# Performance work log

Measured on AMD Instinct MI355X. Metric: run time of the kernel, lower is better.

Reference implementation:

```python
import jax, jax.numpy as jnp
import numpy as np

B, S, DM, H = 4, 2048, 512, 8
HD = DM // H


def setup_inputs() -> dict:
    key = jax.random.key(0)
    ks = jax.random.split(key, 12)
    x = jax.random.normal(ks[0], (B, S, DM), dtype=jnp.float32)
    # causal lower-triangular mask [B, S, S]
    mask = jnp.broadcast_to(jnp.tril(jnp.ones((S, S), dtype=jnp.int32)), (B, S, S))
    # sorted irregular day offsets (trading-day-like), in days
    days_offset = jnp.sort(
        jax.random.uniform(ks[1], (B, S), dtype=jnp.float32) * 3000.0, axis=-1
    )
    scale = 1.0 / np.sqrt(DM)
    Wq = jax.random.normal(ks[2], (DM, DM), dtype=jnp.float32) * scale
    bq = jnp.zeros((DM,), dtype=jnp.float32)
    Wk = jax.random.normal(ks[3], (DM, DM), dtype=jnp.float32) * scale
    bk = jnp.zeros((DM,), dtype=jnp.float32)
    Wv = jax.random.normal(ks[4], (DM, DM), dtype=jnp.float32) * scale
    bv = jnp.zeros((DM,), dtype=jnp.float32)
    Wo = jax.random.normal(ks[5], (DM, DM), dtype=jnp.float32) * scale
    bo = jnp.zeros((DM,), dtype=jnp.float32)
    decay_rate = jnp.float32(0.1)
    return {
        "x": x, "mask": mask, "days_offset": days_offset,
        "Wq": Wq, "bq": bq, "Wk": Wk, "bk": bk,
        "Wv": Wv, "bv": bv, "Wo": Wo, "bo": bo,
        "decay_rate": decay_rate,
    }


def reference(x, mask, days_offset, Wq, bq, Wk, bk, Wv, bv, Wo, bo, decay_rate):
    b, s, _ = x.shape
    # projections (torch Linear: x @ W.T + b), split heads -> [b, h, s, hd]
    def proj(W, bias):
        return (x @ W.T + bias).reshape(b, s, H, HD).transpose(0, 2, 1, 3)
    q, k, v = proj(Wq, bq), proj(Wk, bk), proj(Wv, bv)
    scores = jnp.einsum("bhqd,bhkd->bhqk", q, k) / jnp.sqrt(jnp.float32(HD))
    # temporal decay: exp(-rate * |t_i - t_j|), broadcast over heads
    dist = jnp.abs(days_offset[:, :, None] - days_offset[:, None, :])  # [b,s,s]
    decay = jnp.exp(-decay_rate * dist)
    scores = scores * decay[:, None, :, :]
    scores = jnp.where(mask[:, None, :, :] == 0, -jnp.inf, scores)
    attn = jax.nn.softmax(scores, axis=-1)  # dropout p=0 (eval)
    out = jnp.einsum("bhqk,bhkd->bhqd", attn, v)
    out = out.transpose(0, 2, 1, 3).reshape(b, s, DM)
    return out @ Wo.T + bo
```

## Files before the change

### kernel.cpp

```cpp
#include <hip/hip_runtime.h>
#include <hip/hip_fp16.h>


#define S_LEN 2048
#define DMODEL 512
#define NH 8
#define HD 64

typedef _Float16 half8 __attribute__((ext_vector_type(8)));
typedef _Float16 half4 __attribute__((ext_vector_type(4)));
typedef float floatx4 __attribute__((ext_vector_type(4)));

__device__ __forceinline__ void gload16(const _Float16* g, _Float16* l) {
    __builtin_amdgcn_global_load_lds(
        (const __attribute__((address_space(1))) void*)g,
        (__attribute__((address_space(3))) void*)l, 16, 0, 0);
}

__device__ __forceinline__ half8 cvt8(float4 a, float4 b) {
    half8 h;
    h[0] = (_Float16)a.x; h[1] = (_Float16)a.y; h[2] = (_Float16)a.z; h[3] = (_Float16)a.w;
    h[4] = (_Float16)b.x; h[5] = (_Float16)b.y; h[6] = (_Float16)b.z; h[7] = (_Float16)b.w;
    return h;
}

__device__ __forceinline__ void stage_f32(
    const float* __restrict__ src, _Float16* __restrict__ dstbase,
    int row, int sw, int lane7, int kcol)
{
    const float* p = src + (size_t)row * DMODEL + kcol + sw * 8;
    float4 a = *(const float4*)p;
    float4 b = *(const float4*)(p + 4);
    *(half8*)(dstbase + row * 64 + lane7 * 8) = cvt8(a, b);
}

__global__ __launch_bounds__(256) void qkv_gemm(
    const float* __restrict__ x,
    const float* __restrict__ Wq, const float* __restrict__ Wk, const float* __restrict__ Wv,
    const float* __restrict__ bq, const float* __restrict__ bk, const float* __restrict__ bv,
    _Float16* __restrict__ outh)
{
    __shared__ _Float16 As[2][128 * 64];
    __shared__ _Float16 Ws[2][128 * 64];
    const int t = threadIdx.x;
    const int bm = blockIdx.x, bn = blockIdx.y, z = blockIdx.z;
    const float* Wp = (z == 0) ? Wq : (z == 1) ? Wk : Wv;
    const float* bias = (z == 0) ? bq : (z == 1) ? bk : bv;
    const int w = t >> 6, lane = t & 63, l15 = lane & 15, quad = lane >> 4;
    const int wrow = (w >> 1) * 64, wcol = (w & 1) * 64;
    const int lrow = lane >> 3, lane7 = lane & 7;
    const int sw = lane7 ^ lrow;
    const float* xb = x  + (size_t)(bm * 128) * DMODEL;
    const float* Wb = Wp + (size_t)(bn * 128) * DMODEL;

    auto stage = [&](int kb, int buf) {
        #pragma unroll
        for (int i = 0; i < 4; ++i) {
            int row = w * 32 + i * 8 + lrow;
            stage_f32(xb, As[buf], row, sw, lane7, kb * 64);
            stage_f32(Wb, Ws[buf], row, sw, lane7, kb * 64);
        }
    };

    floatx4 acc[4][4] = {};
    stage(0, 0);
    for (int kb = 0; kb < 8; ++kb) {
        const int buf = kb & 1;
        __syncthreads();
        if (kb < 7) stage(kb + 1, buf ^ 1);
        #pragma unroll
        for (int kk = 0; kk < 2; ++kk) {
            half8 xf[4], wf[4];
            #pragma unroll
            for (int mt = 0; mt < 4; ++mt)
                xf[mt] = *(const half8*)(&As[buf][(wrow + mt * 16 + l15) * 64 + (((quad + 4 * kk) ^ (l15 & 7)) * 8)]);
            #pragma unroll
            for (int nt = 0; nt < 4; ++nt)
                wf[nt] = *(const half8*)(&Ws[buf][(wcol + nt * 16 + l15) * 64 + (((quad + 4 * kk) ^ (l15 & 7)) * 8)]);
            if (z == 2) {
                #pragma unroll
                for (int mt = 0; mt < 4; ++mt)
                    #pragma unroll
                    for (int nt = 0; nt < 4; ++nt)
                        acc[mt][nt] = __builtin_amdgcn_mfma_f32_16x16x32_f16(xf[mt], wf[nt], acc[mt][nt], 0, 0, 0);
            } else {
                #pragma unroll
                for (int nt = 0; nt < 4; ++nt)
                    #pragma unroll
                    for (int mt = 0; mt < 4; ++mt)
                        acc[nt][mt] = __builtin_amdgcn_mfma_f32_16x16x32_f16(wf[nt], xf[mt], acc[nt][mt], 0, 0, 0);
            }
        }
    }

    if (z == 2) {
        #pragma unroll
        for (int mt = 0; mt < 4; ++mt)
            #pragma unroll
            for (int nt = 0; nt < 4; ++nt) {
                int n = bn * 128 + wcol + nt * 16 + l15;
                float bvv = bias[n];
                int m0 = bm * 128 + wrow + mt * 16 + quad * 4;
                int b = m0 >> 11, s0 = m0 & 2047;
                int hh = n >> 6, hd = n & 63;
                half4 hv;
                #pragma unroll
                for (int r = 0; r < 4; ++r) hv[r] = (_Float16)(acc[mt][nt][r] + bvv);
                *(half4*)(outh + (size_t)2 * (8192 * 512) +
                          ((size_t)(b * NH + hh) * HD + hd) * S_LEN + s0) = hv;
            }
    } else {
        #pragma unroll
        for (int nt = 0; nt < 4; ++nt)
            #pragma unroll
            for (int mt = 0; mt < 4; ++mt) {
                int n0 = bn * 128 + wcol + nt * 16 + quad * 4;
                float4 b4 = *(const float4*)(bias + n0);
                int m = bm * 128 + wrow + mt * 16 + l15;
                int b = m >> 11, s = m & 2047;
                int hh = n0 >> 6, hd0 = n0 & 63;
                half4 hv;
                hv[0] = (_Float16)(acc[nt][mt][0] + b4.x);
                hv[1] = (_Float16)(acc[nt][mt][1] + b4.y);
                hv[2] = (_Float16)(acc[nt][mt][2] + b4.z);
                hv[3] = (_Float16)(acc[nt][mt][3] + b4.w);
                *(half4*)(outh + (size_t)z * (8192 * 512) +
                          ((size_t)(b * NH + hh) * S_LEN + s) * HD + hd0) = hv;
            }
    }
}

__global__ __launch_bounds__(256) void out_gemm(
    const _Float16* __restrict__ A, const float* __restrict__ Wo,
    const float* __restrict__ bo, float* __restrict__ outf)
{
    __shared__ _Float16 As[2][64 * 64];
    __shared__ _Float16 Ws[2][128 * 64];
    const int t = threadIdx.x;
    const int bm = blockIdx.x, bn = blockIdx.y;
    const int w = t >> 6, lane = t & 63, l15 = lane & 15, quad = lane >> 4;
    const int wn = w * 32;
    const int lrow = lane >> 3, lane7 = lane & 7;
    const int sw = lane7 ^ lrow;
    const _Float16* Ab = A  + (size_t)(bm * 64) * DMODEL;
    const float*    Wb = Wo + (size_t)(bn * 128) * DMODEL;

    auto stage = [&](int kb, int buf) {
        #pragma unroll
        for (int i = 0; i < 2; ++i) {
            int row = (w * 2 + i) * 8 + lrow;
            gload16(Ab + (size_t)row * DMODEL + kb * 64 + sw * 8, &As[buf][row * 64]);
        }
        #pragma unroll
        for (int i = 0; i < 4; ++i)
            stage_f32(Wb, Ws[buf], w * 32 + i * 8 + lrow, sw, lane7, kb * 64);
    };

    floatx4 acc[2][4] = {};
    stage(0, 0);
    for (int kb = 0; kb < 8; ++kb) {
        const int buf = kb & 1;
        __syncthreads();
        if (kb < 7) stage(kb + 1, buf ^ 1);
        #pragma unroll
        for (int kk = 0; kk < 2; ++kk) {
            half8 wf[2], af[4];
            #pragma unroll
            for (int nt = 0; nt < 2; ++nt)
                wf[nt] = *(const half8*)(&Ws[buf][(wn + nt * 16 + l15) * 64 + (((quad + 4 * kk) ^ (l15 & 7)) * 8)]);
            #pragma unroll
            for (int mt = 0; mt < 4; ++mt)
                af[mt] = *(const half8*)(&As[buf][(mt * 16 + l15) * 64 + (((quad + 4 * kk) ^ (l15 & 7)) * 8)]);
            #pragma unroll
            for (int nt = 0; nt < 2; ++nt)
                #pragma unroll
                for (int mt = 0; mt < 4; ++mt)
                    acc[nt][mt] = __builtin_amdgcn_mfma_f32_16x16x32_f16(wf[nt], af[mt], acc[nt][mt], 0, 0, 0);
        }
    }

    #pragma unroll
    for (int nt = 0; nt < 2; ++nt)
        #pragma unroll
        for (int mt = 0; mt < 4; ++mt) {
            int n0 = bn * 128 + wn + nt * 16 + quad * 4;
            float4 b4 = *(const float4*)(bo + n0);
            int m = bm * 64 + mt * 16 + l15;
            float4 v;
            v.x = acc[nt][mt][0] + b4.x; v.y = acc[nt][mt][1] + b4.y;
            v.z = acc[nt][mt][2] + b4.z; v.w = acc[nt][mt][3] + b4.w;
            *(float4*)(outf + (size_t)m * DMODEL + n0) = v;
        }
}

__global__ __launch_bounds__(256, 3) void attn_k(
    const _Float16* __restrict__ Qh, const _Float16* __restrict__ Kh,
    const _Float16* __restrict__ Vt, const float* __restrict__ days,
    const float* __restrict__ rate_p, _Float16* __restrict__ Ah)
{
    __shared__ _Float16 Ks[2][64 * 64];
    __shared__ _Float16 Vs[2][64 * 64];
    __shared__ float    eks[2][64];
    __shared__ float4   PsRaw[1024];
    __shared__ float    lred[2][2][64];

    _Float16* Ps  = (_Float16*)PsRaw;
    float*    PsF = (float*)PsRaw;

    const int h = blockIdx.x, b = blockIdx.z;
    const int j = 31 - blockIdx.y;
    const int t = threadIdx.x, w = t >> 6, lane = t & 63;
    const int l15 = lane & 15, quad = lane >> 4, e7 = l15 & 7;
    const int qh = w & 1, kh = w >> 1;
    const float rate = rate_p[0];
    const size_t bhoff = (size_t)(b * NH + h) * (size_t)(S_LEN * HD);
    const _Float16* Qb = Qh + bhoff;
    const _Float16* Kb = Kh + bhoff;
    const _Float16* Vb = Vt + bhoff;
    const float* daysb = days + b * S_LEN;
    const int lrow = lane >> 3, sw = (lane & 7) ^ lrow;

    auto stage = [&](int kt, int buf) {
        #pragma unroll
        for (int i = 0; i < 2; ++i) {
            int grp = w * 2 + i;
            int row = grp * 8 + lrow;
            gload16(Kb + (size_t)(kt * 64 + row) * HD + sw * 8, &Ks[buf][grp * 512]);
            gload16(Vb + (size_t)row * S_LEN + kt * 64 + sw * 8, &Vs[buf][grp * 512]);
        }
        if (w == 0) {
            float tk0 = daysb[kt * 64];
            float d = daysb[kt * 64 + lane];
            eks[buf][lane] = __expf(fminf(rate * (d - tk0), 80.f));
        }
    };

    const int q0 = j * 64 + qh * 32;
    half8 qf[2][2];
    #pragma unroll
    for (int qc = 0; qc < 2; ++qc)
        #pragma unroll
        for (int kk = 0; kk < 2; ++kk)
            qf[qc][kk] = *(const half8*)(Qb + (size_t)(q0 + qc * 16 + l15) * HD + kk * 32 + quad * 8);

    const int   qg[2] = {q0 + l15, q0 + 16 + l15};
    const float tq[2] = {daysb[qg[0]], daysb[qg[1]]};

    floatx4 oacc[2][4] = {};
    float lacc[2] = {0.f, 0.f};

    floatx4 scA[2][2], scB[2][2];
    half8  vfA[4], vfB[4];
    floatx4 ekA[2], ekB[2];
    float  eqA[2], eqB[2];

    auto load_tile = [&](int kt, int par, floatx4 (&sc)[2][2], half8 (&vf)[4],
                         floatx4 (&ek)[2], float (&eq)[2]) {
        half8 kf[2][2];
        #pragma unroll
        for (int c = 0; c < 2; ++c) {
            const int C = kh * 2 + c;
            #pragma unroll
            for (int kk = 0; kk < 2; ++kk)
                kf[c][kk] = *(const half8*)(&Ks[par][(C * 16 + l15) * 64 + (((quad + 4 * kk) ^ e7) * 8)]);
        }
        #pragma unroll
        for (int qc = 0; qc < 2; ++qc)
            #pragma unroll
            for (int c = 0; c < 2; ++c) {
                floatx4 z = {};
                z = __builtin_amdgcn_mfma_f32_16x16x32_f16(kf[c][0], qf[qc][0], z, 0, 0, 0);
                sc[qc][c] = __builtin_amdgcn_mfma_f32_16x16x32_f16(kf[c][1], qf[qc][1], z, 0, 0, 0);
            }
        #pragma unroll
        for (int s4 = 0; s4 < 4; ++s4)
            vf[s4] = *(const half8*)(&Vs[par][(s4 * 16 + l15) * 64 + (((quad + 4 * kh) ^ e7) * 8)]);
        const float tk0 = daysb[kt * 64];
        #pragma unroll
        for (int qc = 0; qc < 2; ++qc)
            eq[qc] = 0.125f * __expf(-rate * (tq[qc] - tk0));
        #pragma unroll
        for (int c = 0; c < 2; ++c)
            ek[c] = *(const floatx4*)(&eks[par][kh * 32 + c * 16 + quad * 4]);
    };

    auto softmax_pv = [&](floatx4 (&sc)[2][2], half8 (&vf)[4],
                          floatx4 (&ek)[2], float (&eq)[2], bool dg, int kt) {
        #pragma unroll
        for (int qc = 0; qc < 2; ++qc)
            #pragma unroll
            for (int c = 0; c < 2; ++c) {
                float pv[4];
                #pragma unroll
                for (int r = 0; r < 4; ++r) {
                    float p = __expf(sc[qc][c][r] * (eq[qc] * ek[c][r]));
                    if (dg && (kt * 64 + kh * 32 + c * 16 + quad * 4 + r) > qg[qc]) p = 0.f;
                    lacc[qc] += p;
                    pv[r] = p;
                }
                half4 hv;
                hv[0] = (_Float16)pv[0]; hv[1] = (_Float16)pv[1];
                hv[2] = (_Float16)pv[2]; hv[3] = (_Float16)pv[3];
                *(half4*)(&Ps[(w * 2 + qc) * 1024 + l15 * 64 +
                              (((kh * 4 + 2 * c + (quad >> 1)) ^ e7) * 8) + (quad & 1) * 4]) = hv;
            }
        #pragma unroll
        for (int qc = 0; qc < 2; ++qc) {
            half8 pf = *(const half8*)(&Ps[(w * 2 + qc) * 1024 + l15 * 64 + (((quad + 4 * kh) ^ e7) * 8)]);
            #pragma unroll
            for (int s4 = 0; s4 < 4; ++s4)
                oacc[qc][s4] = __builtin_amdgcn_mfma_f32_16x16x32_f16(vf[s4], pf, oacc[qc][s4], 0, 0, 0);
        }
    };

    stage(0, 0);
    __syncthreads();
    if (j > 0) stage(1, 1);
    load_tile(0, 0, scA, vfA, ekA, eqA);

    int kt = 1;
    for (; kt + 1 <= j; kt += 2) {
        const int p1 = kt & 1;
        __syncthreads();
        if (kt < j) stage(kt + 1, p1 ^ 1);
        load_tile(kt, p1, scB, vfB, ekB, eqB);
        softmax_pv(scA, vfA, ekA, eqA, false, kt - 1);
        const int p2 = p1 ^ 1;
        __syncthreads();
        if (kt + 1 < j) stage(kt + 2, p2 ^ 1);
        load_tile(kt + 1, p2, scA, vfA, ekA, eqA);
        softmax_pv(scB, vfB, ekB, eqB, false, kt);
    }
    if (kt <= j) {
        const int p1 = kt & 1;
        __syncthreads();
        load_tile(kt, p1, scB, vfB, ekB, eqB);
        softmax_pv(scA, vfA, ekA, eqA, false, kt - 1);
        softmax_pv(scB, vfB, ekB, eqB, true, j);
    } else {
        softmax_pv(scA, vfA, ekA, eqA, true, j);
    }

    __syncthreads();
    if (w >= 2) {
        #pragma unroll
        for (int qc = 0; qc < 2; ++qc) {
            #pragma unroll
            for (int s4 = 0; s4 < 4; ++s4)
                *(floatx4*)(&PsF[(((w & 1) * 2 + qc) * 4 + s4) * 256 + lane * 4]) = oacc[qc][s4];
            lred[w & 1][qc][lane] = lacc[qc];
        }
    }
    __syncthreads();
    if (w < 2) {
        #pragma unroll
        for (int qc = 0; qc < 2; ++qc) {
            float l = lacc[qc] + lred[w][qc][lane];
            l += __shfl_xor(l, 16);
            l += __shfl_xor(l, 32);
            const float linv = 1.0f / l;
            #pragma unroll
            for (int s4 = 0; s4 < 4; ++s4) {
                floatx4 o = oacc[qc][s4] +
                    *(const floatx4*)(&PsF[((w * 2 + qc) * 4 + s4) * 256 + lane * 4]);
                half4 hv;
                #pragma unroll
                for (int r = 0; r < 4; ++r) hv[r] = (_Float16)(o[r] * linv);
                *(half4*)(Ah + ((size_t)(b * S_LEN) + qg[qc]) * DMODEL + h * HD + s4 * 16 + quad * 4) = hv;
            }
        }
    }
}

extern "C" void kernel_launch(void* const* d_in, const int* in_sizes, int n_in,
                              void* d_out, int out_size, void* d_ws, size_t ws_size,
                              hipStream_t stream)
{
    const float* x    = (const float*)d_in[0];
    const float* days = (const float*)d_in[2];
    const float* Wq   = (const float*)d_in[3];
    const float* bq   = (const float*)d_in[4];
    const float* Wk   = (const float*)d_in[5];
    const float* bk   = (const float*)d_in[6];
    const float* Wv   = (const float*)d_in[7];
    const float* bv   = (const float*)d_in[8];
    const float* Wo   = (const float*)d_in[9];
    const float* bo   = (const float*)d_in[10];
    const float* rate = (const float*)d_in[11];
    float* out = (float*)d_out;

    _Float16* Qh = (_Float16*)d_ws;
    _Float16* Kh = Qh + 4194304;
    _Float16* Vh = Kh + 4194304;
    _Float16* Ah = Vh + 4194304;

    dim3 g0(64, 4, 3);
    qkv_gemm<<<g0, 256, 0, stream>>>(x, Wq, Wk, Wv, bq, bk, bv, Qh);

    dim3 ga(NH, 32, 4);
    attn_k<<<ga, 256, 0, stream>>>(Qh, Kh, Vh, days, rate, Ah);

    dim3 g1(128, 4, 1);
    out_gemm<<<g1, 4 * 64, 0, stream>>>(Ah, Wo, bo, out);
}
```

Measured before the change: 218.2 us.

## Pre-cast inputs to fp16, use async LDS loads, pair causal attention tiles

```diff
diff --git a/kernel.cpp b/kernel.cpp
--- a/kernel.cpp
+++ b/kernel.cpp
@@ -17,26 +17,34 @@
         (__attribute__((address_space(3))) void*)l, 16, 0, 0);
 }
 
-__device__ __forceinline__ half8 cvt8(float4 a, float4 b) {
-    half8 h;
-    h[0] = (_Float16)a.x; h[1] = (_Float16)a.y; h[2] = (_Float16)a.z; h[3] = (_Float16)a.w;
-    h[4] = (_Float16)b.x; h[5] = (_Float16)b.y; h[6] = (_Float16)b.z; h[7] = (_Float16)b.w;
-    return h;
-}
-
-__device__ __forceinline__ void stage_f32(
-    const float* __restrict__ src, _Float16* __restrict__ dstbase,
-    int row, int sw, int lane7, int kcol)
+__global__ __launch_bounds__(256) void cast_f2h(
+    const float* __restrict__ x,
+    const float* __restrict__ Wq, const float* __restrict__ Wk,
+    const float* __restrict__ Wv, const float* __restrict__ Wo,
+    _Float16* __restrict__ xh, _Float16* __restrict__ Wh)
 {
-    const float* p = src + (size_t)row * DMODEL + kcol + sw * 8;
-    float4 a = *(const float4*)p;
-    float4 b = *(const float4*)(p + 4);
-    *(half8*)(dstbase + row * 64 + lane7 * 8) = cvt8(a, b);
+    const int z = blockIdx.y;
+    const float* src;
+    _Float16* dst;
+    int n;
+    if (z == 0) { src = x; dst = xh; n = 8192 * 512; }
+    else {
+        src = (z == 1) ? Wq : (z == 2) ? Wk : (z == 3) ? Wv : Wo;
+        dst = Wh + (z - 1) * 262144;
+        n = 262144;
+    }
+    const int stride = gridDim.x * 256 * 4;
+    for (int i = (blockIdx.x * 256 + threadIdx.x) * 4; i < n; i += stride) {
+        float4 v = *(const float4*)(src + i);
+        half4 h;
+        h[0] = (_Float16)v.x; h[1] = (_Float16)v.y;
+        h[2] = (_Float16)v.z; h[3] = (_Float16)v.w;
+        *(half4*)(dst + i) = h;
+    }
 }
 
 __global__ __launch_bounds__(256) void qkv_gemm(
-    const float* __restrict__ x,
-    const float* __restrict__ Wq, const float* __restrict__ Wk, const float* __restrict__ Wv,
+    const _Float16* __restrict__ xh, const _Float16* __restrict__ Wh,
     const float* __restrict__ bq, const float* __restrict__ bk, const float* __restrict__ bv,
     _Float16* __restrict__ outh)
 {
@@ -44,21 +52,21 @@
     __shared__ _Float16 Ws[2][128 * 64];
     const int t = threadIdx.x;
     const int bm = blockIdx.x, bn = blockIdx.y, z = blockIdx.z;
-    const float* Wp = (z == 0) ? Wq : (z == 1) ? Wk : Wv;
     const float* bias = (z == 0) ? bq : (z == 1) ? bk : bv;
     const int w = t >> 6, lane = t & 63, l15 = lane & 15, quad = lane >> 4;
     const int wrow = (w >> 1) * 64, wcol = (w & 1) * 64;
     const int lrow = lane >> 3, lane7 = lane & 7;
     const int sw = lane7 ^ lrow;
-    const float* xb = x  + (size_t)(bm * 128) * DMODEL;
-    const float* Wb = Wp + (size_t)(bn * 128) * DMODEL;
+    const _Float16* xb = xh + (size_t)(bm * 128) * DMODEL;
+    const _Float16* Wb = Wh + z * 262144 + (size_t)(bn * 128) * DMODEL;
 
     auto stage = [&](int kb, int buf) {
         #pragma unroll
         for (int i = 0; i < 4; ++i) {
-            int row = w * 32 + i * 8 + lrow;
-            stage_f32(xb, As[buf], row, sw, lane7, kb * 64);
-            stage_f32(Wb, Ws[buf], row, sw, lane7, kb * 64);
+            const int grp = w * 4 + i;
+            const int row = grp * 8 + lrow;
+            gload16(xb + (size_t)row * DMODEL + kb * 64 + sw * 8, &As[buf][grp * 512]);
+            gload16(Wb + (size_t)row * DMODEL + kb * 64 + sw * 8, &Ws[buf][grp * 512]);
         }
     };
 
@@ -131,7 +139,7 @@
 }
 
 __global__ __launch_bounds__(256) void out_gemm(
-    const _Float16* __restrict__ A, const float* __restrict__ Wo,
+    const _Float16* __restrict__ A, const _Float16* __restrict__ Woh,
     const float* __restrict__ bo, float* __restrict__ outf)
 {
     __shared__ _Float16 As[2][64 * 64];
@@ -142,18 +150,22 @@
     const int wn = w * 32;
     const int lrow = lane >> 3, lane7 = lane & 7;
     const int sw = lane7 ^ lrow;
-    const _Float16* Ab = A  + (size_t)(bm * 64) * DMODEL;
-    const float*    Wb = Wo + (size_t)(bn * 128) * DMODEL;
+    const _Float16* Ab = A   + (size_t)(bm * 64) * DMODEL;
+    const _Float16* Wb = Woh + (size_t)(bn * 128) * DMODEL;
 
     auto stage = [&](int kb, int buf) {
         #pragma unroll
         for (int i = 0; i < 2; ++i) {
-            int row = (w * 2 + i) * 8 + lrow;
-            gload16(Ab + (size_t)row * DMODEL + kb * 64 + sw * 8, &As[buf][row * 64]);
-        }
-        #pragma unroll
-        for (int i = 0; i < 4; ++i)
-            stage_f32(Wb, Ws[buf], w * 32 + i * 8 + lrow, sw, lane7, kb * 64);
+            const int grp = w * 2 + i;
+            const int row = grp * 8 + lrow;
+            gload16(Ab + (size_t)row * DMODEL + kb * 64 + sw * 8, &As[buf][grp * 512]);
+        }
+        #pragma unroll
+        for (int i = 0; i < 4; ++i) {
+            const int grp = w * 4 + i;
+            const int row = grp * 8 + lrow;
+            gload16(Wb + (size_t)row * DMODEL + kb * 64 + sw * 8, &Ws[buf][grp * 512]);
+        }
     };
 
     floatx4 acc[2][4] = {};
@@ -193,7 +205,7 @@
         }
 }
 
-__global__ __launch_bounds__(256, 3) void attn_k(
+__global__ __launch_bounds__(256, 2) void attn_k(
     const _Float16* __restrict__ Qh, const _Float16* __restrict__ Kh,
     const _Float16* __restrict__ Vt, const float* __restrict__ days,
     const float* __restrict__ rate_p, _Float16* __restrict__ Ah)
@@ -207,8 +219,7 @@
     _Float16* Ps  = (_Float16*)PsRaw;
     float*    PsF = (float*)PsRaw;
 
-    const int h = blockIdx.x, b = blockIdx.z;
-    const int j = 31 - blockIdx.y;
+    const int h = blockIdx.x, pr = blockIdx.y, b = blockIdx.z;
     const int t = threadIdx.x, w = t >> 6, lane = t & 63;
     const int l15 = lane & 15, quad = lane >> 4, e7 = l15 & 7;
     const int qh = w & 1, kh = w >> 1;
@@ -235,141 +246,150 @@
         }
     };
 
-    const int q0 = j * 64 + qh * 32;
-    half8 qf[2][2];
-    #pragma unroll
-    for (int qc = 0; qc < 2; ++qc)
-        #pragma unroll
-        for (int kk = 0; kk < 2; ++kk)
-            qf[qc][kk] = *(const half8*)(Qb + (size_t)(q0 + qc * 16 + l15) * HD + kk * 32 + quad * 8);
-
-    const int   qg[2] = {q0 + l15, q0 + 16 + l15};
-    const float tq[2] = {daysb[qg[0]], daysb[qg[1]]};
-
-    floatx4 oacc[2][4] = {};
-    float lacc[2] = {0.f, 0.f};
-
-    floatx4 scA[2][2], scB[2][2];
-    half8  vfA[4], vfB[4];
-    floatx4 ekA[2], ekB[2];
-    float  eqA[2], eqB[2];
-
-    auto load_tile = [&](int kt, int par, floatx4 (&sc)[2][2], half8 (&vf)[4],
-                         floatx4 (&ek)[2], float (&eq)[2]) {
-        half8 kf[2][2];
-        #pragma unroll
-        for (int c = 0; c < 2; ++c) {
-            const int C = kh * 2 + c;
+    auto run_phase = [&](int j, int par0, int nextj) -> int {
+        const int q0 = j * 64 + qh * 32;
+        half8 qf[2][2];
+        #pragma unroll
+        for (int qc = 0; qc < 2; ++qc)
             #pragma unroll
             for (int kk = 0; kk < 2; ++kk)
-                kf[c][kk] = *(const half8*)(&Ks[par][(C * 16 + l15) * 64 + (((quad + 4 * kk) ^ e7) * 8)]);
-        }
-        #pragma unroll
-        for (int qc = 0; qc < 2; ++qc)
+                qf[qc][kk] = *(const half8*)(Qb + (size_t)(q0 + qc * 16 + l15) * HD + kk * 32 + quad * 8);
+
+        const int   qg[2] = {q0 + l15, q0 + 16 + l15};
+        const float tq[2] = {daysb[qg[0]], daysb[qg[1]]};
+
+        floatx4 oacc[2][4] = {};
+        float lacc[2] = {0.f, 0.f};
+
+        floatx4 scA[2][2], scB[2][2];
+        half8  vfA[4], vfB[4];
+        floatx4 ekA[2], ekB[2];
+        float  eqA[2], eqB[2];
+
+        auto load_tile = [&](int kt, int par, floatx4 (&sc)[2][2], half8 (&vf)[4],
+                             floatx4 (&ek)[2], float (&eq)[2]) {
+            half8 kf[2][2];
             #pragma unroll
             for (int c = 0; c < 2; ++c) {
-                floatx4 z = {};
-                z = __builtin_amdgcn_mfma_f32_16x16x32_f16(kf[c][0], qf[qc][0], z, 0, 0, 0);
-                sc[qc][c] = __builtin_amdgcn_mfma_f32_16x16x32_f16(kf[c][1], qf[qc][1], z, 0, 0, 0);
-            }
-        #pragma unroll
-        for (int s4 = 0; s4 < 4; ++s4)
-            vf[s4] = *(const half8*)(&Vs[par][(s4 * 16 + l15) * 64 + (((quad + 4 * kh) ^ e7) * 8)]);
-        const float tk0 = daysb[kt * 64];
-        #pragma unroll
-        for (int qc = 0; qc < 2; ++qc)
-            eq[qc] = 0.125f * __expf(-rate * (tq[qc] - tk0));
-        #pragma unroll
-        for (int c = 0; c < 2; ++c)
-            ek[c] = *(const floatx4*)(&eks[par][kh * 32 + c * 16 + quad * 4]);
+                const int C = kh * 2 + c;
+                #pragma unroll
+                for (int kk = 0; kk < 2; ++kk)
+                    kf[c][kk] = *(const half8*)(&Ks[par][(C * 16 + l15) * 64 + (((quad + 4 * kk) ^ e7) * 8)]);
+            }
+            #pragma unroll
+            for (int qc = 0; qc < 2; ++qc)
+                #pragma unroll
+                for (int c = 0; c < 2; ++c) {
+                    floatx4 z = {};
+                    z = __builtin_amdgcn_mfma_f32_16x16x32_f16(kf[c][0], qf[qc][0], z, 0, 0, 0);
+                    sc[qc][c] = __builtin_amdgcn_mfma_f32_16x16x32_f16(kf[c][1], qf[qc][1], z, 0, 0, 0);
+                }
+            #pragma unroll
+            for (int s4 = 0; s4 < 4; ++s4)
+                vf[s4] = *(const half8*)(&Vs[par][(s4 * 16 + l15) * 64 + (((quad + 4 * kh) ^ e7) * 8)]);
+            const float tk0 = daysb[kt * 64];
+            #pragma unroll
+            for (int qc = 0; qc < 2; ++qc)
+                eq[qc] = 0.125f * __expf(-rate * (tq[qc] - tk0));
+            #pragma unroll
+            for (int c = 0; c < 2; ++c)
+                ek[c] = *(const floatx4*)(&eks[par][kh * 32 + c * 16 + quad * 4]);
+        };
+
+        auto softmax_pv = [&](floatx4 (&sc)[2][2], half8 (&vf)[4],
+                              floatx4 (&ek)[2], float (&eq)[2], bool dg, int kt) {
+            #pragma unroll
+            for (int qc = 0; qc < 2; ++qc)
+                #pragma unroll
+                for (int c = 0; c < 2; ++c) {
+                    float pv[4];
+                    #pragma unroll
+                    for (int r = 0; r < 4; ++r) {
+                        float p = __expf(sc[qc][c][r] * (eq[qc] * ek[c][r]));
+                        if (dg && (kt * 64 + kh * 32 + c * 16 + quad * 4 + r) > qg[qc]) p = 0.f;
+                        lacc[qc] += p;
+                        pv[r] = p;
+                    }
+                    half4 hv;
+                    hv[0] = (_Float16)pv[0]; hv[1] = (_Float16)pv[1];
+                    hv[2] = (_Float16)pv[2]; hv[3] = (_Float16)pv[3];
+                    *(half4*)(&Ps[(w * 2 + qc) * 1024 + l15 * 64 +
+                                  (((kh * 4 + 2 * c + (quad >> 1)) ^ e7) * 8) + (quad & 1) * 4]) = hv;
+                }
+            #pragma unroll
+            for (int qc = 0; qc < 2; ++qc) {
+                half8 pf = *(const half8*)(&Ps[(w * 2 + qc) * 1024 + l15 * 64 + (((quad + 4 * kh) ^ e7) * 8)]);
+                #pragma unroll
+                for (int s4 = 0; s4 < 4; ++s4)
+                    oacc[qc][s4] = __builtin_amdgcn_mfma_f32_16x16x32_f16(vf[s4], pf, oacc[qc][s4], 0, 0, 0);
+            }
+        };
+
+        __syncthreads();
+        if (j > 0) stage(1, par0 ^ 1);
+        load_tile(0, par0, scA, vfA, ekA, eqA);
+
+        int kt = 1;
+        for (; kt + 1 <= j; kt += 2) {
+            const int p1 = (par0 + kt) & 1;
+            __syncthreads();
+            if (kt < j) stage(kt + 1, p1 ^ 1);
+            load_tile(kt, p1, scB, vfB, ekB, eqB);
+            softmax_pv(scA, vfA, ekA, eqA, false, kt - 1);
+            const int p2 = p1 ^ 1;
+            __syncthreads();
+            if (kt + 1 < j) stage(kt + 2, p2 ^ 1);
+            load_tile(kt + 1, p2, scA, vfA, ekA, eqA);
+            softmax_pv(scB, vfB, ekB, eqB, false, kt);
+        }
+        if (kt <= j) {
+            const int p1 = (par0 + kt) & 1;
+            __syncthreads();
+            load_tile(kt, p1, scB, vfB, ekB, eqB);
+            softmax_pv(scA, vfA, ekA, eqA, false, kt - 1);
+            softmax_pv(scB, vfB, ekB, eqB, true, j);
+        } else {
+            softmax_pv(scA, vfA, ekA, eqA, true, j);
+        }
+
+        __syncthreads();
+        if (w >= 2) {
+            #pragma unroll
+            for (int qc = 0; qc < 2; ++qc) {
+                #pragma unroll
+                for (int s4 = 0; s4 < 4; ++s4)
+                    *(floatx4*)(&PsF[(((w & 1) * 2 + qc) * 4 + s4) * 256 + lane * 4]) = oacc[qc][s4];
+                lred[w & 1][qc][lane] = lacc[qc];
+            }
+        }
+        __syncthreads();
+        const int parNext = (par0 + j + 1) & 1;
+        if (nextj >= 0) stage(0, parNext);
+        if (w < 2) {
+            #pragma unroll
+            for (int qc = 0; qc < 2; ++qc) {
+                float l = lacc[qc] + lred[w][qc][lane];
+                l += __shfl_xor(l, 16);
+                l += __shfl_xor(l, 32);
+                const float linv = 1.0f / l;
+                #pragma unroll
+                for (int s4 = 0; s4 < 4; ++s4) {
+                    floatx4 o = oacc[qc][s4] +
+                        *(const floatx4*)(&PsF[((w * 2 + qc) * 4 + s4) * 256 + lane * 4]);
+                    half4 hv;
+                    #pragma unroll
+                    for (int r = 0; r < 4; ++r) hv[r] = (_Float16)(o[r] * linv);
+                    *(half4*)(Ah + ((size_t)(b * S_LEN) + qg[qc]) * DMODEL + h * HD + s4 * 16 + quad * 4) = hv;
+                }
+            }
+        }
+        return parNext;
     };
 
-    auto softmax_pv = [&](floatx4 (&sc)[2][2], half8 (&vf)[4],
-                          floatx4 (&ek)[2], float (&eq)[2], bool dg, int kt) {
-        #pragma unroll
-        for (int qc = 0; qc < 2; ++qc)
-            #pragma unroll
-            for (int c = 0; c < 2; ++c) {
-                float pv[4];
-                #pragma unroll
-                for (int r = 0; r < 4; ++r) {
-                    float p = __expf(sc[qc][c][r] * (eq[qc] * ek[c][r]));
-                    if (dg && (kt * 64 + kh * 32 + c * 16 + quad * 4 + r) > qg[qc]) p = 0.f;
-                    lacc[qc] += p;
-                    pv[r] = p;
-                }
-                half4 hv;
-                hv[0] = (_Float16)pv[0]; hv[1] = (_Float16)pv[1];
-                hv[2] = (_Float16)pv[2]; hv[3] = (_Float16)pv[3];
-                *(half4*)(&Ps[(w * 2 + qc) * 1024 + l15 * 64 +
-                              (((kh * 4 + 2 * c + (quad >> 1)) ^ e7) * 8) + (quad & 1) * 4]) = hv;
-            }
-        #pragma unroll
-        for (int qc = 0; qc < 2; ++qc) {
-            half8 pf = *(const half8*)(&Ps[(w * 2 + qc) * 1024 + l15 * 64 + (((quad + 4 * kh) ^ e7) * 8)]);
-            #pragma unroll
-            for (int s4 = 0; s4 < 4; ++s4)
-                oacc[qc][s4] = __builtin_amdgcn_mfma_f32_16x16x32_f16(vf[s4], pf, oacc[qc][s4], 0, 0, 0);
-        }
-    };
-
+    const int j0 = pr, j1 = 31 - pr;
     stage(0, 0);
-    __syncthreads();
-    if (j > 0) stage(1, 1);
-    load_tile(0, 0, scA, vfA, ekA, eqA);
-
-    int kt = 1;
-    for (; kt + 1 <= j; kt += 2) {
-        const int p1 = kt & 1;
-        __syncthreads();
-        if (kt < j) stage(kt + 1, p1 ^ 1);
-        load_tile(kt, p1, scB, vfB, ekB, eqB);
-        softmax_pv(scA, vfA, ekA, eqA, false, kt - 1);
-        const int p2 = p1 ^ 1;
-        __syncthreads();
-        if (kt + 1 < j) stage(kt + 2, p2 ^ 1);
-        load_tile(kt + 1, p2, scA, vfA, ekA, eqA);
-        softmax_pv(scB, vfB, ekB, eqB, false, kt);
-    }
-    if (kt <= j) {
-        const int p1 = kt & 1;
-        __syncthreads();
-        load_tile(kt, p1, scB, vfB, ekB, eqB);
-        softmax_pv(scA, vfA, ekA, eqA, false, kt - 1);
-        softmax_pv(scB, vfB, ekB, eqB, true, j);
-    } else {
-        softmax_pv(scA, vfA, ekA, eqA, true, j);
-    }
-
-    __syncthreads();
-    if (w >= 2) {
-        #pragma unroll
-        for (int qc = 0; qc < 2; ++qc) {
-            #pragma unroll
-            for (int s4 = 0; s4 < 4; ++s4)
-                *(floatx4*)(&PsF[(((w & 1) * 2 + qc) * 4 + s4) * 256 + lane * 4]) = oacc[qc][s4];
-            lred[w & 1][qc][lane] = lacc[qc];
-        }
-    }
-    __syncthreads();
-    if (w < 2) {
-        #pragma unroll
-        for (int qc = 0; qc < 2; ++qc) {
-            float l = lacc[qc] + lred[w][qc][lane];
-            l += __shfl_xor(l, 16);
-            l += __shfl_xor(l, 32);
-            const float linv = 1.0f / l;
-            #pragma unroll
-            for (int s4 = 0; s4 < 4; ++s4) {
-                floatx4 o = oacc[qc][s4] +
-                    *(const floatx4*)(&PsF[((w * 2 + qc) * 4 + s4) * 256 + lane * 4]);
-                half4 hv;
-                #pragma unroll
-                for (int r = 0; r < 4; ++r) hv[r] = (_Float16)(o[r] * linv);
-                *(half4*)(Ah + ((size_t)(b * S_LEN) + qg[qc]) * DMODEL + h * HD + s4 * 16 + quad * 4) = hv;
-            }
-        }
-    }
+    int p1 = run_phase(j0, 0, j1);
+    run_phase(j1, p1, -1);
 }
 
 extern "C" void kernel_launch(void* const* d_in, const int* in_sizes, int n_in,
@@ -389,17 +409,21 @@
     const float* rate = (const float*)d_in[11];
     float* out = (float*)d_out;
 
-    _Float16* Qh = (_Float16*)d_ws;
-    _Float16* Kh = Qh + 4194304;
-    _Float16* Vh = Kh + 4194304;
-    _Float16* Ah = Vh + 4194304;
+    _Float16* Qh  = (_Float16*)d_ws;
+    _Float16* Kh  = Qh + 4194304;
+    _Float16* Vh  = Kh + 4194304;
+    _Float16* AhX = Vh + 4194304;
+    _Float16* Wh  = AhX + 4194304;
+
+    dim3 gc(512, 5, 1);
+    cast_f2h<<<gc, 256, 0, stream>>>(x, Wq, Wk, Wv, Wo, AhX, Wh);
 
     dim3 g0(64, 4, 3);
-    qkv_gemm<<<g0, 256, 0, stream>>>(x, Wq, Wk, Wv, bq, bk, bv, Qh);
-
-    dim3 ga(NH, 32, 4);
-    attn_k<<<ga, 256, 0, stream>>>(Qh, Kh, Vh, days, rate, Ah);
+    qkv_gemm<<<g0, 256, 0, stream>>>(AhX, Wh, bq, bk, bv, Qh);
+
+    dim3 ga(NH, 16, 4);
+    attn_k<<<ga, 256, 0, stream>>>(Qh, Kh, Vh, days, rate, AhX);
 
     dim3 g1(128, 4, 1);
-    out_gemm<<<g1, 4 * 64, 0, stream>>>(Ah, Wo, bo, out);
-}
+    out_gemm<<<g1, 256, 0, stream>>>(AhX, Wh + 3 * 262144, bo, out);
+}
```

New measurement: 203.3 us. -6.8%, faster.
